# Kernel optimization log

Hardware: AMD Instinct MI355X
Metric: run time of the kernel (lower is better)

The kernel has to match this reference:

```python
import jax, jax.numpy as jnp
import numpy as np

T, B = 16, 32
C, H, W = 3, 120, 160
NET, LSTM_H, AC_H, NACT = 512, 512, 512, 8
CONV_OUT = 64 * 11 * 16  # 11264, from 120x160 through k[8,4,3]/s[4,2,1]


def setup_inputs() -> dict:
    key = jax.random.key(0)
    ks = jax.random.split(key, 32)
    rn = lambda k, shape, s=0.05: jax.random.normal(k, shape, jnp.float32) * s
    return {
        "x": jax.random.normal(ks[0], (T * B, C, H, W), jnp.float32),
        "done": jax.random.randint(ks[1], (T * B,), 0, 2, jnp.int32),
        "h0": rn(ks[2], (1, B, LSTM_H), 1.0),
        "c0": rn(ks[3], (1, B, LSTM_H), 1.0),
        "w1": rn(ks[4], (32, C, 8, 8)), "b1": jnp.zeros((32,), jnp.float32),
        "w2": rn(ks[5], (64, 32, 4, 4)), "b2": jnp.zeros((64,), jnp.float32),
        "w3": rn(ks[6], (64, 64, 3, 3)), "b3": jnp.zeros((64,), jnp.float32),
        "fcW": rn(ks[7], (NET, CONV_OUT), 0.01), "fcb": jnp.zeros((NET,), jnp.float32),
        "Wih": rn(ks[8], (4 * LSTM_H, NET)), "Whh": rn(ks[9], (4 * LSTM_H, LSTM_H)),
        "bih": jnp.zeros((4 * LSTM_H,), jnp.float32), "bhh": jnp.zeros((4 * LSTM_H,), jnp.float32),
        "A1": rn(ks[10], (AC_H, LSTM_H)), "Ab1": jnp.zeros((AC_H,), jnp.float32),
        "A2": rn(ks[11], (NACT, AC_H)), "Ab2": jnp.zeros((NACT,), jnp.float32),
        "C1": rn(ks[12], (AC_H, LSTM_H)), "Cb1": jnp.zeros((AC_H,), jnp.float32),
        "C2": rn(ks[13], (1, AC_H)), "Cb2": jnp.zeros((1,), jnp.float32),
    }


DN = ("NCHW", "OIHW", "NCHW")


def _conv(x, w, b, s):
    y = jax.lax.conv_general_dilated(x, w, (s, s), "VALID", dimension_numbers=DN)
    return y + b[None, :, None, None]


def reference(x, done, h0, c0, w1, b1, w2, b2, w3, b3, fcW, fcb,
              Wih, Whh, bih, bhh, A1, Ab1, A2, Ab2, C1, Cb1, C2, Cb2):
    # CNN feature extractor
    h = jax.nn.relu(_conv(x, w1, b1, 4))
    h = jax.nn.relu(_conv(h, w2, b2, 2))
    h = jax.nn.relu(_conv(h, w3, b3, 1))
    h = h.reshape(h.shape[0], -1)                     # [T*B, CONV_OUT]
    h = jax.nn.leaky_relu(h @ fcW.T + fcb, 0.2)       # [T*B, NET]

    bsz = h0.shape[1]
    xs = h.reshape(-1, bsz, Wih.shape[1])             # [T, B, NET]
    d = done.astype(h.dtype).reshape(-1, bsz)         # [T, B]

    def step(carry, inp):
        hs, cs = carry
        xt, dt = inp
        m = (1.0 - dt)[:, None]                       # done-mask reset
        hs, cs = hs * m, cs * m
        g = xt @ Wih.T + bih + hs @ Whh.T + bhh       # [B, 4H], gate order i,f,g,o
        i, f, gg, o = jnp.split(g, 4, axis=-1)
        cs = jax.nn.sigmoid(f) * cs + jax.nn.sigmoid(i) * jnp.tanh(gg)
        hs = jax.nn.sigmoid(o) * jnp.tanh(cs)
        return (hs, cs), hs

    (hT, cT), outs = jax.lax.scan(step, (h0[0], c0[0]), (xs, d))
    nh = outs.reshape(-1, outs.shape[-1])             # [T*B, LSTM_H]

    a = jax.nn.leaky_relu(nh @ A1.T + Ab1, 0.01)
    logits = a @ A2.T + Ab2                           # [T*B, NACT]
    v = jax.nn.leaky_relu(nh @ C1.T + Cb1, 0.01)
    value = v @ C2.T + Cb2                            # [T*B, 1]
    return logits, value, hT[None], cT[None]
```

## Files before the change

### kernel.cpp

```cpp
#include <hip/hip_runtime.h>
#include <hip/hip_bf16.h>
#include <math.h>

using short8 = __attribute__((ext_vector_type(8))) short;
using f32x4  = __attribute__((ext_vector_type(4))) float;
typedef unsigned long long u64;

#define MFMA16(a, b, c) __builtin_amdgcn_mfma_f32_16x16x32_bf16(a, b, c, 0, 0, 0)

__device__ __forceinline__ short f2bs(float f) {
    __hip_bfloat16 h = __float2bfloat16(f);
    return __builtin_bit_cast(short, h);
}
__device__ __forceinline__ float bs2f(short s) {
    return __uint_as_float(((unsigned)(unsigned short)s) << 16);
}

__global__ void __launch_bounds__(256) k_megaprep(
        const float* __restrict__ w1, const float* __restrict__ w2,
        const float* __restrict__ w3, const float* __restrict__ fcW,
        const float* __restrict__ Wih, const float* __restrict__ Whh,
        const float* __restrict__ A1, const float* __restrict__ C1,
        const float* __restrict__ A2, const float* __restrict__ C2,
        const float* __restrict__ h0, const int* __restrict__ done,
        const float* __restrict__ bih, const float* __restrict__ bhh,
        const float* __restrict__ Ab1, const float* __restrict__ Cb1,
        short* __restrict__ wc1, short* __restrict__ wc2, short* __restrict__ wc3,
        short* __restrict__ fcwr, short* __restrict__ wihb, short* __restrict__ whhb,
        short* __restrict__ a1b, short* __restrict__ c1b, short* __restrict__ a2b,
        short* __restrict__ c2b, short* __restrict__ hm0,
        float* __restrict__ bias2, float* __restrict__ biasAC, unsigned* __restrict__ flags) {
    __shared__ short t[176 * 76];
    const int bid = blockIdx.x, tid = threadIdx.x;

    auto cvt4 = [&](const float* in, short* out, int i) {
        float4 v = *(const float4*)(in + i * 4);
        out[i * 4 + 0] = f2bs(v.x); out[i * 4 + 1] = f2bs(v.y);
        out[i * 4 + 2] = f2bs(v.z); out[i * 4 + 3] = f2bs(v.w);
    };

    if (bid < 512) {
        int r = bid;
        for (int it = 0; it < 11; ++it) {
            int c4 = it * 256 + tid;
            float4 v = *(const float4*)(fcW + (size_t)r * 11264 + c4 * 4);
            int c = c4 * 4;
            int oc = c / 176, pix = c % 176;
            t[(pix + 0) * 76 + oc] = f2bs(v.x);
            t[(pix + 1) * 76 + oc] = f2bs(v.y);
            t[(pix + 2) * 76 + oc] = f2bs(v.z);
            t[(pix + 3) * 76 + oc] = f2bs(v.w);
        }
        __syncthreads();
        for (int it = 0; it < 6; ++it) {
            int j8 = it * 256 + tid;
            if (j8 < 1408) {
                int j = j8 * 8, pix = j >> 6, oc0 = j & 63;
                const short* tp = &t[pix * 76 + oc0];
                short8 v;
                ((uint2*)&v)[0] = *(const uint2*)tp;
                ((uint2*)&v)[1] = *(const uint2*)(tp + 4);
                *(short8*)&fcwr[(size_t)r * 11264 + j] = v;
            }
        }
    } else if (bid < 1536) {
        cvt4(Wih, wihb, (bid - 512) * 256 + tid);
    } else if (bid < 2560) {
        cvt4(Whh, whhb, (bid - 1536) * 256 + tid);
    } else if (bid < 2816) {
        cvt4(A1, a1b, (bid - 2560) * 256 + tid);
    } else if (bid < 3072) {
        cvt4(C1, c1b, (bid - 2816) * 256 + tid);
    } else if (bid < 3078) {
        cvt4(w1, wc1, (bid - 3072) * 256 + tid);
    } else if (bid < 3206) {
        int i = (bid - 3078) * 256 + tid;
        int oc = i >> 9, col = i & 511;
        int kh = col >> 7, kw = (col >> 5) & 3, ic = col & 31;
        wc2[i] = f2bs(w2[((oc * 32 + ic) * 4 + kh) * 4 + kw]);
    } else if (bid < 3350) {
        int i = (bid - 3206) * 256 + tid;
        int oc = i / 576, col = i % 576;
        int kh = col / 192, r = col % 192, kw = r >> 6, ic = r & 63;
        wc3[i] = f2bs(w3[((oc * 64 + ic) * 3 + kh) * 3 + kw]);
    } else if (bid < 3354) {
        cvt4(A2, a2b, (bid - 3350) * 256 + tid);
    } else if (bid < 3355) {
        if (tid < 128) cvt4(C2, c2b, tid);
    } else if (bid < 3419) {
        int i = (bid - 3355) * 256 + tid;
        float m = 1.f - (float)done[i >> 9];
        hm0[i] = f2bs(h0[i] * m);
    } else if (bid < 3427) {
        int i = (bid - 3419) * 256 + tid;
        bias2[i] = bih[i] + bhh[i];
    } else if (bid < 3431) {
        int i = (bid - 3427) * 256 + tid;
        biasAC[i] = (i < 512) ? Ab1[i] : Cb1[i - 512];
    } else {
        if (tid < 16) flags[tid] = 0u;
    }
}

__global__ void __launch_bounds__(256) k_conv123(
        const float* __restrict__ x,   const short* __restrict__ Wc1,
        const float* __restrict__ b1,
        const short* __restrict__ Wc2, const float* __restrict__ b2,
        const short* __restrict__ Wc3, const float* __restrict__ b3,
        short* __restrict__ y3) {
    __shared__ short img1[36192];
    __shared__ short img2[14976];
    __shared__ short ct[2048];
    const int n = blockIdx.x, tid = threadIdx.x;
    const int w = tid >> 6, l = tid & 63, lr = l & 15, lg = l >> 4;
    const int par = w >> 1, nfh = w & 1;

    {
        short8 bf[6][2];
#pragma unroll
        for (int ks = 0; ks < 6; ++ks)
#pragma unroll
            for (int nf = 0; nf < 2; ++nf)
                bf[ks][nf] = *(const short8*)&Wc1[(nf * 16 + lr) * 192 + ks * 32 + lg * 8];
        const float bc0 = b1[lr], bc1 = b1[16 + lr];
        const float* xb = x + (size_t)n * 57600;
        auto tileBase = [&](int tt) -> const float* {
            int p = tt * 16 + lr; if (p > 1130) p = 1130;
            int oh = p / 39, ow = p - oh * 39;
            return xb + (oh * 4) * 160 + ow * 4;
        };
        const int ntiles = (w == 3) ? 17 : 18;
        float4 fA[6][2], fB[6][2];
        {
            const float* base = tileBase(w);
#pragma unroll
            for (int ks = 0; ks < 6; ++ks) {
                int ic = ks >> 1, kh = (ks & 1) * 4 + lg;
                const float* ap = base + ic * 19200 + kh * 160;
                fA[ks][0] = *(const float4*)ap;
                fA[ks][1] = *(const float4*)(ap + 4);
            }
        }
        for (int i = 0; i < ntiles; ++i) {
            const int tt = i * 4 + w;
            if (i + 1 < ntiles) {
                const float* nb = tileBase(tt + 4);
#pragma unroll
                for (int ks = 0; ks < 6; ++ks) {
                    int ic = ks >> 1, kh = (ks & 1) * 4 + lg;
                    const float* ap = nb + ic * 19200 + kh * 160;
                    fB[ks][0] = *(const float4*)ap;
                    fB[ks][1] = *(const float4*)(ap + 4);
                }
            }
            f32x4 acc[2] = {};
#pragma unroll
            for (int ks = 0; ks < 6; ++ks) {
                short8 a;
                a[0] = f2bs(fA[ks][0].x); a[1] = f2bs(fA[ks][0].y);
                a[2] = f2bs(fA[ks][0].z); a[3] = f2bs(fA[ks][0].w);
                a[4] = f2bs(fA[ks][1].x); a[5] = f2bs(fA[ks][1].y);
                a[6] = f2bs(fA[ks][1].z); a[7] = f2bs(fA[ks][1].w);
                acc[0] = MFMA16(a, bf[ks][0], acc[0]);
                acc[1] = MFMA16(a, bf[ks][1], acc[1]);
            }
#pragma unroll
            for (int j = 0; j < 4; ++j) {
                ct[w * 512 + (lg * 4 + j) * 32 + lr] = f2bs(fmaxf(acc[0][j] + bc0, 0.f));
                ct[w * 512 + (lg * 4 + j) * 32 + 16 + lr] = f2bs(fmaxf(acc[1][j] + bc1, 0.f));
            }
            asm volatile("s_waitcnt lgkmcnt(0)" ::: "memory");
            {
                int row = l >> 2, c8 = (l & 3) * 8;
                int pg = tt * 16 + row;
                if (pg < 1131) {
                    short8 v = *(const short8*)&ct[w * 512 + row * 32 + c8];
                    int b = pg * 64 + c8 * 2;
                    b ^= ((b >> 7) & 7) << 4;
                    *(short8*)((char*)img1 + b) = v;
                }
            }
            asm volatile("s_waitcnt lgkmcnt(0)" ::: "memory");
            if (i + 1 < ntiles) {
#pragma unroll
                for (int ks = 0; ks < 6; ++ks) {
                    fA[ks][0] = fB[ks][0];
                    fA[ks][1] = fB[ks][1];
                }
            }
        }
    }
    __syncthreads();

    {
        short8 bfg[16][2];
#pragma unroll
        for (int ks = 0; ks < 16; ++ks)
#pragma unroll
            for (int q2 = 0; q2 < 2; ++q2)
                bfg[ks][q2] = *(const short8*)&Wc2[(nfh * 32 + q2 * 16 + lr) * 512 + ks * 32 + lg * 8];
        float bc[2] = {b2[nfh * 32 + lr], b2[nfh * 32 + 16 + lr]};
        for (int t = par; t < 16; t += 2) {
            int p = t * 16 + lr;
            int pc = p < 234 ? p : 233;
            int oh = pc / 18, ow = pc - oh * 18;
            int base = (oh * 2 * 39 + ow * 2) * 64 + lg * 16;
            f32x4 acc[2] = {};
#pragma unroll
            for (int ks = 0; ks < 16; ++ks) {
                int kh = ks >> 2, kw = ks & 3;
                int b = base + (kh * 39 + kw) * 64;
                b ^= ((b >> 7) & 7) << 4;
                short8 a = *(const short8*)((const char*)img1 + b);
                acc[0] = MFMA16(a, bfg[ks][0], acc[0]);
                acc[1] = MFMA16(a, bfg[ks][1], acc[1]);
            }
#pragma unroll
            for (int q2 = 0; q2 < 2; ++q2)
#pragma unroll
                for (int j = 0; j < 4; ++j)
                    ct[par * 1024 + (lg * 4 + j) * 64 + nfh * 32 + q2 * 16 + lr] =
                        f2bs(fmaxf(acc[q2][j] + bc[q2], 0.f));
            __syncthreads();
            int li = nfh * 64 + l;
            int row = li >> 3, c8 = (li & 7) * 8;
            short8 v = *(const short8*)&ct[par * 1024 + row * 64 + c8];
            int pg = t * 16 + row;
            if (pg < 234) {
                int b = (pg * 64 + c8) * 2;
                b ^= ((b >> 7) & 7) << 4;
                *(short8*)((char*)img2 + b) = v;
            }
            __syncthreads();
        }
    }
    __syncthreads();

    {
        short8 bfg[18][2];
#pragma unroll
        for (int ks = 0; ks < 18; ++ks)
#pragma unroll
            for (int q2 = 0; q2 < 2; ++q2)
                bfg[ks][q2] = *(const short8*)&Wc3[(nfh * 32 + q2 * 16 + lr) * 576 + ks * 32 + lg * 8];
        float bc[2] = {b3[nfh * 32 + lr], b3[nfh * 32 + 16 + lr]};
        for (int t = par; t < 12; t += 2) {
            int p = t * 16 + lr;
            int pc = p < 176 ? p : 175;
            int oh = pc >> 4, ow = pc & 15;
            int base = (oh * 18 + ow) * 128 + lg * 16;
            f32x4 acc[2] = {};
#pragma unroll
            for (int ks = 0; ks < 18; ++ks) {
                int kh = ks / 6, r6 = ks % 6, kw = r6 >> 1, ich = r6 & 1;
                int b = base + (kh * 18 + kw) * 128 + ich * 64;
                b ^= ((b >> 7) & 7) << 4;
                short8 a = *(const short8*)((const char*)img2 + b);
                acc[0] = MFMA16(a, bfg[ks][0], acc[0]);
                acc[1] = MFMA16(a, bfg[ks][1], acc[1]);
            }
#pragma unroll
            for (int q2 = 0; q2 < 2; ++q2)
#pragma unroll
                for (int j = 0; j < 4; ++j)
                    ct[par * 1024 + (lg * 4 + j) * 64 + nfh * 32 + q2 * 16 + lr] =
                        f2bs(fmaxf(acc[q2][j] + bc[q2], 0.f));
            __syncthreads();
            int li = nfh * 64 + l;
            int row = li >> 3, c8 = (li & 7) * 8;
            short8 v = *(const short8*)&ct[par * 1024 + row * 64 + c8];
            int pg = t * 16 + row;
            if (pg < 176)
                *(short8*)&y3[((size_t)n * 176 + pg) * 64 + c8] = v;
            __syncthreads();
        }
    }
}

__global__ void k_gemm_mfma(const short* __restrict__ A, const short* __restrict__ W,
                            float* __restrict__ part, int M, int N, int K, int kPerSplit) {
    __shared__ short As[2][64 * 40];
    __shared__ short Ws[2][64 * 40];
    const int tid = threadIdx.x;
    const int m0 = blockIdx.y * 64, n0 = blockIdx.x * 64;
    const int k0s = blockIdx.z * kPerSplit, k0e = k0s + kPerSplit;
    const int w = tid >> 6, l = tid & 63;
    const int wr = w >> 1, wc = w & 1;
    const int sr = tid >> 2, sc = tid & 3;
    const int lr = l & 15, lg = l >> 4;
    f32x4 acc[2][2] = {};
    for (int k0 = k0s; k0 < k0e; k0 += 64) {
        short8 av0 = *(const short8*)(A + (size_t)(m0 + sr) * K + k0 + sc * 8);
        short8 av1 = *(const short8*)(A + (size_t)(m0 + sr) * K + k0 + 32 + sc * 8);
        short8 wv0 = *(const short8*)(W + (size_t)(n0 + sr) * K + k0 + sc * 8);
        short8 wv1 = *(const short8*)(W + (size_t)(n0 + sr) * K + k0 + 32 + sc * 8);
        __syncthreads();
        *(short8*)&As[0][sr * 40 + sc * 8] = av0;
        *(short8*)&As[1][sr * 40 + sc * 8] = av1;
        *(short8*)&Ws[0][sr * 40 + sc * 8] = wv0;
        *(short8*)&Ws[1][sr * 40 + sc * 8] = wv1;
        __syncthreads();
        int cb = lg * 8;
#pragma unroll
        for (int h = 0; h < 2; ++h) {
            short8 a0 = *(const short8*)&As[h][(wr * 32 + lr) * 40 + cb];
            short8 a1 = *(const short8*)&As[h][(wr * 32 + 16 + lr) * 40 + cb];
            short8 b0 = *(const short8*)&Ws[h][(wc * 32 + lr) * 40 + cb];
            short8 b1 = *(const short8*)&Ws[h][(wc * 32 + 16 + lr) * 40 + cb];
            acc[0][0] = MFMA16(a0, b0, acc[0][0]);
            acc[0][1] = MFMA16(a0, b1, acc[0][1]);
            acc[1][0] = MFMA16(a1, b0, acc[1][0]);
            acc[1][1] = MFMA16(a1, b1, acc[1][1]);
        }
    }
    float* pp = part + (size_t)blockIdx.z * M * N;
#pragma unroll
    for (int mi = 0; mi < 2; ++mi)
#pragma unroll
        for (int ni = 0; ni < 2; ++ni)
#pragma unroll
            for (int j = 0; j < 4; ++j) {
                int row = m0 + wr * 32 + mi * 16 + lg * 4 + j;
                int col = n0 + wc * 32 + ni * 16 + lr;
                pp[(size_t)row * N + col] = acc[mi][ni][j];
            }
}

__global__ void k_epilogue(const float* __restrict__ part, const float* __restrict__ bias,
                           short* __restrict__ out_b, float* __restrict__ out_f,
                           int MN, int N, int S, float slope) {
    int i = (blockIdx.x * 256 + threadIdx.x) * 4;
    if (i >= MN) return;
    float4 v = *(const float4*)(part + i);
    for (int s = 1; s < S; ++s) {
        float4 p = *(const float4*)(part + (size_t)s * MN + i);
        v.x += p.x; v.y += p.y; v.z += p.z; v.w += p.w;
    }
    float4 b = *(const float4*)(bias + (i % N));
    v.x += b.x; v.y += b.y; v.z += b.z; v.w += b.w;
    v.x = (v.x >= 0.f) ? v.x : v.x * slope;
    v.y = (v.y >= 0.f) ? v.y : v.y * slope;
    v.z = (v.z >= 0.f) ? v.z : v.z * slope;
    v.w = (v.w >= 0.f) ? v.w : v.w * slope;
    if (out_b) {
        out_b[i + 0] = f2bs(v.x); out_b[i + 1] = f2bs(v.y);
        out_b[i + 2] = f2bs(v.z); out_b[i + 3] = f2bs(v.w);
    }
    if (out_f) *(float4*)(out_f + i) = v;
}

__global__ void k_gemm_bias(const short* __restrict__ A, const short* __restrict__ W,
                            const float* __restrict__ bias, short* __restrict__ out_b,
                            float* __restrict__ out_f, int M, int N, int K, float slope) {
    __shared__ short As[2][64 * 40];
    __shared__ short Ws[2][64 * 40];
    const int tid = threadIdx.x;
    const int m0 = blockIdx.y * 64, n0 = blockIdx.x * 64;
    const int w = tid >> 6, l = tid & 63;
    const int wr = w >> 1, wc = w & 1;
    const int sr = tid >> 2, sc = tid & 3;
    const int lr = l & 15, lg = l >> 4;
    f32x4 acc[2][2] = {};
    for (int k0 = 0; k0 < K; k0 += 64) {
        short8 av0 = *(const short8*)(A + (size_t)(m0 + sr) * K + k0 + sc * 8);
        short8 av1 = *(const short8*)(A + (size_t)(m0 + sr) * K + k0 + 32 + sc * 8);
        short8 wv0 = *(const short8*)(W + (size_t)(n0 + sr) * K + k0 + sc * 8);
        short8 wv1 = *(const short8*)(W + (size_t)(n0 + sr) * K + k0 + 32 + sc * 8);
        __syncthreads();
        *(short8*)&As[0][sr * 40 + sc * 8] = av0;
        *(short8*)&As[1][sr * 40 + sc * 8] = av1;
        *(short8*)&Ws[0][sr * 40 + sc * 8] = wv0;
        *(short8*)&Ws[1][sr * 40 + sc * 8] = wv1;
        __syncthreads();
        int cb = lg * 8;
#pragma unroll
        for (int h = 0; h < 2; ++h) {
            short8 a0 = *(const short8*)&As[h][(wr * 32 + lr) * 40 + cb];
            short8 a1 = *(const short8*)&As[h][(wr * 32 + 16 + lr) * 40 + cb];
            short8 b0 = *(const short8*)&Ws[h][(wc * 32 + lr) * 40 + cb];
            short8 b1 = *(const short8*)&Ws[h][(wc * 32 + 16 + lr) * 40 + cb];
            acc[0][0] = MFMA16(a0, b0, acc[0][0]);
            acc[0][1] = MFMA16(a0, b1, acc[0][1]);
            acc[1][0] = MFMA16(a1, b0, acc[1][0]);
            acc[1][1] = MFMA16(a1, b1, acc[1][1]);
        }
    }
#pragma unroll
    for (int mi = 0; mi < 2; ++mi)
#pragma unroll
        for (int ni = 0; ni < 2; ++ni)
#pragma unroll
            for (int j = 0; j < 4; ++j) {
                int row = m0 + wr * 32 + mi * 16 + lg * 4 + j;
                int col = n0 + wc * 32 + ni * 16 + lr;
                float v = acc[mi][ni][j] + bias[col];
                v = (v >= 0.f) ? v : v * slope;
                if (out_f) out_f[(size_t)row * N + col] = v;
                else       out_b[(size_t)row * N + col] = f2bs(v);
            }
}

__global__ void __launch_bounds__(1024) k_lstm_all4(
        const float* __restrict__ P, const short* __restrict__ Whhb,
        const int* __restrict__ done, u64* __restrict__ hq0, u64* __restrict__ hq1,
        const float* __restrict__ c0, short* __restrict__ nh,
        float* __restrict__ outH, float* __restrict__ outC, unsigned* __restrict__ flags) {
    __shared__ short hs[32 * 520];
    __shared__ float gb[4 * 32 * 33];
    __shared__ short ch[32 * 33];
    const int b = blockIdx.x;
    const int tid = threadIdx.x;
    const int w = tid >> 6, l = tid & 63, lr = l & 15, lg = l >> 4;
    const int mt = w & 1, nt = w >> 1;
    const int r = nt * 16 + lr;
    const int gate = r >> 5, ul = r & 31;
    const int G = gate * 512 + b * 32 + ul;
    short8 bfg[16];
    const short* wrow = Whhb + (size_t)G * 512;
#pragma unroll
    for (int ks = 0; ks < 16; ++ks) bfg[ks] = *(const short8*)(wrow + ks * 32 + lg * 8);
    const int cu = tid >> 5, cb = tid & 31;
    float cr = c0[cb * 512 + b * 32 + cu];
    const int pb = tid >> 3;
    unsigned dmC = 0, dmP = 0;
#pragma unroll
    for (int q = 0; q < 16; ++q) {
        dmC |= (done[q * 32 + cb] ? 1u : 0u) << q;
        dmP |= (done[q * 32 + pb] ? 1u : 0u) << q;
    }
    float pr[4];
#pragma unroll
    for (int j = 0; j < 4; ++j)
        pr[j] = P[(size_t)(mt * 16 + lg * 4 + j) * 2048 + G];

    for (int t = 0; t < 16; ++t) {
        const u64* hin = (t & 1) ? hq1 : hq0;
        u64* hout      = (t & 1) ? hq0 : hq1;
        if (t > 0) {
            if (tid < 16) {
                while (__hip_atomic_load(flags + tid, __ATOMIC_RELAXED,
                                         __HIP_MEMORY_SCOPE_AGENT) < (unsigned)t)
                    __builtin_amdgcn_s_sleep(1);
            }
            __syncthreads();
        }
#pragma unroll
        for (int it = 0; it < 4; ++it) {
            int i = it * 1024 + tid;
            u64 g = __hip_atomic_load(hin + i, __ATOMIC_RELAXED, __HIP_MEMORY_SCOPE_AGENT);
            *(u64*)&hs[(i >> 7) * 520 + (i & 127) * 4] = g;
        }
        __syncthreads();
        f32x4 acc = {};
#pragma unroll
        for (int ks = 0; ks < 16; ++ks) {
            short8 a = *(const short8*)&hs[(mt * 16 + lr) * 520 + ks * 32 + lg * 8];
            acc = MFMA16(a, bfg[ks], acc);
        }
#pragma unroll
        for (int j = 0; j < 4; ++j)
            gb[gate * 1056 + ul * 33 + (mt * 16 + lg * 4 + j)] = acc[j] + pr[j];
        __syncthreads();
        {
            float gi = gb[0 * 1056 + cu * 33 + cb];
            float gf = gb[1 * 1056 + cu * 33 + cb];
            float gg = gb[2 * 1056 + cu * 33 + cb];
            float go = gb[3 * 1056 + cu * 33 + cb];
            float m = ((dmC >> t) & 1u) ? 0.f : 1.f;
            float ig = 1.f / (1.f + expf(-gi));
            float fg = 1.f / (1.f + expf(-gf));
            float gt = tanhf(gg);
            float og = 1.f / (1.f + expf(-go));
            float cn = fg * (cr * m) + ig * gt;
            float hn = og * tanhf(cn);
            cr = cn;
            ch[cu * 33 + cb] = f2bs(hn);
            if (t == 15) {
                outH[cb * 512 + b * 32 + cu] = hn;
                outC[cb * 512 + b * 32 + cu] = cn;
            }
        }
        __syncthreads();
        if (t < 15) {
            if (tid < 256) {
                int bb3 = tid >> 3, uq = (tid & 7) * 4;
                u64 q = 0;
                if (!((dmP >> (t + 1)) & 1u)) {
                    unsigned lo = ((unsigned)(unsigned short)ch[uq * 33 + bb3]) |
                                  (((unsigned)(unsigned short)ch[(uq + 1) * 33 + bb3]) << 16);
                    unsigned hi = ((unsigned)(unsigned short)ch[(uq + 2) * 33 + bb3]) |
                                  (((unsigned)(unsigned short)ch[(uq + 3) * 33 + bb3]) << 16);
                    q = (u64)lo | ((u64)hi << 32);
                }
                __hip_atomic_store(hout + bb3 * 128 + b * 8 + (tid & 7), q,
                                   __ATOMIC_RELAXED, __HIP_MEMORY_SCOPE_AGENT);
            }
            asm volatile("s_waitcnt vmcnt(0)" ::: "memory");
            __syncthreads();
            if (tid == 0)
                __hip_atomic_store(flags + b, (unsigned)(t + 1),
                                   __ATOMIC_RELAXED, __HIP_MEMORY_SCOPE_AGENT);
        }
        if (tid < 512) {
            int bb2 = tid >> 4, up = (tid & 15) * 2;
            unsigned pkv = ((unsigned)(unsigned short)ch[up * 33 + bb2]) |
                           (((unsigned)(unsigned short)ch[(up + 1) * 33 + bb2]) << 16);
            *(unsigned*)&nh[(size_t)(t * 32 + bb2) * 512 + b * 32 + up] = pkv;
        }
        int tp = (t < 15) ? t + 1 : 15;
#pragma unroll
        for (int j = 0; j < 4; ++j)
            pr[j] = P[(size_t)(tp * 32 + mt * 16 + lg * 4 + j) * 2048 + G];
    }
}

__global__ void k_heads(const short* __restrict__ aAC,
                        const short* __restrict__ A2b, const float* __restrict__ Ab2,
                        const short* __restrict__ C2b, const float* __restrict__ Cb2,
                        float* __restrict__ out) {
    int idx = blockIdx.x * 4 + (threadIdx.x >> 6);
    int l = threadIdx.x & 63;
    if (idx >= 4608) return;
    int row = idx / 9, col = idx % 9;
    const short* act = aAC + (size_t)row * 1024 + (col < 8 ? 0 : 512);
    const short* wr  = (col < 8) ? (A2b + (size_t)col * 512) : C2b;
    short8 a = *(const short8*)(act + l * 8);
    short8 wv = *(const short8*)(wr + l * 8);
    float s = 0.f;
#pragma unroll
    for (int q = 0; q < 8; ++q) s += bs2f(a[q]) * bs2f(wv[q]);
#pragma unroll
    for (int off = 32; off > 0; off >>= 1) s += __shfl_xor(s, off, 64);
    if (l == 0) {
        if (col < 8) out[row * 8 + col] = s + Ab2[col];
        else out[4096 + row] = s + Cb2[0];
    }
}


extern "C" void kernel_launch(void* const* d_in, const int* in_sizes, int n_in,
                              void* d_out, int out_size, void* d_ws, size_t ws_size,
                              hipStream_t stream) {
    (void)in_sizes; (void)n_in; (void)out_size; (void)ws_size;
    const float* x    = (const float*)d_in[0];
    const int*   done = (const int*)  d_in[1];
    const float* h0   = (const float*)d_in[2];
    const float* c0   = (const float*)d_in[3];
    const float* w1   = (const float*)d_in[4];
    const float* b1   = (const float*)d_in[5];
    const float* w2   = (const float*)d_in[6];
    const float* b2   = (const float*)d_in[7];
    const float* w3   = (const float*)d_in[8];
    const float* b3   = (const float*)d_in[9];
    const float* fcW  = (const float*)d_in[10];
    const float* fcb  = (const float*)d_in[11];
    const float* Wih  = (const float*)d_in[12];
    const float* Whh  = (const float*)d_in[13];
    const float* bih  = (const float*)d_in[14];
    const float* bhh  = (const float*)d_in[15];
    const float* A1   = (const float*)d_in[16];
    const float* Ab1  = (const float*)d_in[17];
    const float* A2   = (const float*)d_in[18];
    const float* Ab2  = (const float*)d_in[19];
    const float* C1   = (const float*)d_in[20];
    const float* Cb1  = (const float*)d_in[21];
    const float* C2   = (const float*)d_in[22];
    const float* Cb2  = (const float*)d_in[23];
    float* out = (float*)d_out;

    char* wsp = (char*)d_ws;
    auto alloc = [&](size_t bytes) {
        char* p = wsp; wsp += (bytes + 255) & ~(size_t)255; return p;
    };
    short* a3s  = (short*)alloc(5767168ull * 2);
    short* hfc  = (short*)alloc(262144ull * 2);
    float* P    = (float*)alloc(1048576ull * 4);
    short* whhb = (short*)alloc(1048576ull * 2);
    u64*   hq0  = (u64*)  alloc(16384ull * 2);
    u64*   hq1  = (u64*)  alloc(16384ull * 2);
    short* nh   = (short*)alloc(262144ull * 2);
    short* aAC  = (short*)alloc(524288ull * 2);
    float* part = (float*)alloc(2097152ull * 4);
    short* wc1  = (short*)alloc(6144ull * 2);
    short* wc2  = (short*)alloc(32768ull * 2);
    short* wc3  = (short*)alloc(36864ull * 2);
    short* fcwr = (short*)alloc(5767168ull * 2);
    short* wihb = (short*)alloc(1048576ull * 2);
    short* a1b  = (short*)alloc(262144ull * 2);
    short* c1b  = (short*)alloc(262144ull * 2);
    short* a2b  = (short*)alloc(4096ull * 2);
    short* c2b  = (short*)alloc(512ull * 2);
    float* bias2  = (float*)alloc(2048ull * 4);
    float* biasAC = (float*)alloc(1024ull * 4);
    unsigned* flags = (unsigned*)alloc(256);

    k_megaprep<<<3432, 256, 0, stream>>>(w1, w2, w3, fcW, Wih, Whh, A1, C1, A2, C2,
                                         h0, done, bih, bhh, Ab1, Cb1,
                                         wc1, wc2, wc3, fcwr, wihb, whhb,
                                         a1b, c1b, a2b, c2b, (short*)hq0,
                                         bias2, biasAC, flags);

    k_conv123<<<512, 256, 0, stream>>>(x, wc1, b1, wc2, b2, wc3, b3, a3s);

    k_gemm_mfma<<<dim3(8, 8, 8), 256, 0, stream>>>(a3s, fcwr, part, 512, 512, 11264, 1408);
    k_epilogue<<<256, 256, 0, stream>>>(part, fcb, hfc, nullptr, 262144, 512, 8, 0.2f);

    k_gemm_bias<<<dim3(32, 8), 256, 0, stream>>>(hfc, wihb, bias2, nullptr, P,
                                                 512, 2048, 512, 1.0f);

    k_lstm_all4<<<16, 1024, 0, stream>>>(P, whhb, done, hq0, hq1, c0, nh,
                                         out + 4608, out + 20992, flags);

    k_gemm_bias<<<dim3(16, 8), 256, 0, stream>>>(nh, a1b, biasAC, aAC, nullptr,
                                                 512, 1024, 512, 0.01f);
    k_heads<<<1152, 256, 0, stream>>>(aAC, a2b, Ab2, c2b, Cb2, out);
}
```

Baseline: 194.3 us.

## Replace full conv1 LDS image with 16-row ring buffer processed in two phases

Result: slower. 207.4 us (+6.7%).

```diff
diff --git a/kernel.cpp b/kernel.cpp
--- a/kernel.cpp
+++ b/kernel.cpp
@@ -108,31 +108,33 @@
         const short* __restrict__ Wc2, const float* __restrict__ b2,
         const short* __restrict__ Wc3, const float* __restrict__ b3,
         short* __restrict__ y3) {
-    __shared__ short img1[36192];
+    __shared__ short ring[19968];
     __shared__ short img2[14976];
     __shared__ short ct[2048];
     const int n = blockIdx.x, tid = threadIdx.x;
     const int w = tid >> 6, l = tid & 63, lr = l & 15, lg = l >> 4;
     const int par = w >> 1, nfh = w & 1;
 
-    {
-        short8 bf[6][2];
-#pragma unroll
-        for (int ks = 0; ks < 6; ++ks)
-#pragma unroll
-            for (int nf = 0; nf < 2; ++nf)
-                bf[ks][nf] = *(const short8*)&Wc1[(nf * 16 + lr) * 192 + ks * 32 + lg * 8];
-        const float bc0 = b1[lr], bc1 = b1[16 + lr];
-        const float* xb = x + (size_t)n * 57600;
+    short8 bf1[6][2];
+#pragma unroll
+    for (int ks = 0; ks < 6; ++ks)
+#pragma unroll
+        for (int nf = 0; nf < 2; ++nf)
+            bf1[ks][nf] = *(const short8*)&Wc1[(nf * 16 + lr) * 192 + ks * 32 + lg * 8];
+    const float bc10 = b1[lr], bc11 = b1[16 + lr];
+    const float* xb = x + (size_t)n * 57600;
+
+    auto conv1_tiles = [&](int tstart, int tcount) {
         auto tileBase = [&](int tt) -> const float* {
             int p = tt * 16 + lr; if (p > 1130) p = 1130;
             int oh = p / 39, ow = p - oh * 39;
             return xb + (oh * 4) * 160 + ow * 4;
         };
-        const int ntiles = (w == 3) ? 17 : 18;
+        const int nt = (tcount - w + 3) >> 2;
+        if (nt <= 0) return;
         float4 fA[6][2], fB[6][2];
         {
-            const float* base = tileBase(w);
+            const float* base = tileBase(tstart + w);
 #pragma unroll
             for (int ks = 0; ks < 6; ++ks) {
                 int ic = ks >> 1, kh = (ks & 1) * 4 + lg;
@@ -141,9 +143,9 @@
                 fA[ks][1] = *(const float4*)(ap + 4);
             }
         }
-        for (int i = 0; i < ntiles; ++i) {
-            const int tt = i * 4 + w;
-            if (i + 1 < ntiles) {
+        for (int i = 0; i < nt; ++i) {
+            const int tt = tstart + w + i * 4;
+            if (i + 1 < nt) {
                 const float* nb = tileBase(tt + 4);
 #pragma unroll
                 for (int ks = 0; ks < 6; ++ks) {
@@ -161,13 +163,13 @@
                 a[2] = f2bs(fA[ks][0].z); a[3] = f2bs(fA[ks][0].w);
                 a[4] = f2bs(fA[ks][1].x); a[5] = f2bs(fA[ks][1].y);
                 a[6] = f2bs(fA[ks][1].z); a[7] = f2bs(fA[ks][1].w);
-                acc[0] = MFMA16(a, bf[ks][0], acc[0]);
-                acc[1] = MFMA16(a, bf[ks][1], acc[1]);
+                acc[0] = MFMA16(a, bf1[ks][0], acc[0]);
+                acc[1] = MFMA16(a, bf1[ks][1], acc[1]);
             }
 #pragma unroll
             for (int j = 0; j < 4; ++j) {
-                ct[w * 512 + (lg * 4 + j) * 32 + lr] = f2bs(fmaxf(acc[0][j] + bc0, 0.f));
-                ct[w * 512 + (lg * 4 + j) * 32 + 16 + lr] = f2bs(fmaxf(acc[1][j] + bc1, 0.f));
+                ct[w * 512 + (lg * 4 + j) * 32 + lr] = f2bs(fmaxf(acc[0][j] + bc10, 0.f));
+                ct[w * 512 + (lg * 4 + j) * 32 + 16 + lr] = f2bs(fmaxf(acc[1][j] + bc11, 0.f));
             }
             asm volatile("s_waitcnt lgkmcnt(0)" ::: "memory");
             {
@@ -175,13 +177,14 @@
                 int pg = tt * 16 + row;
                 if (pg < 1131) {
                     short8 v = *(const short8*)&ct[w * 512 + row * 32 + c8];
-                    int b = pg * 64 + c8 * 2;
+                    int prow = pg / 39, pcol = pg - prow * 39;
+                    int b = ((prow & 15) * 39 + pcol) * 64 + c8 * 2;
                     b ^= ((b >> 7) & 7) << 4;
-                    *(short8*)((char*)img1 + b) = v;
+                    *(short8*)((char*)ring + b) = v;
                 }
             }
             asm volatile("s_waitcnt lgkmcnt(0)" ::: "memory");
-            if (i + 1 < ntiles) {
+            if (i + 1 < nt) {
 #pragma unroll
                 for (int ks = 0; ks < 6; ++ks) {
                     fA[ks][0] = fB[ks][0];
@@ -189,10 +192,9 @@
                 }
             }
         }
-    }
-    __syncthreads();
-
-    {
+    };
+
+    auto conv2_tiles = [&](int pxbase, int pxlast) {
         short8 bfg[16][2];
 #pragma unroll
         for (int ks = 0; ks < 16; ++ks)
@@ -200,18 +202,18 @@
             for (int q2 = 0; q2 < 2; ++q2)
                 bfg[ks][q2] = *(const short8*)&Wc2[(nfh * 32 + q2 * 16 + lr) * 512 + ks * 32 + lg * 8];
         float bc[2] = {b2[nfh * 32 + lr], b2[nfh * 32 + 16 + lr]};
-        for (int t = par; t < 16; t += 2) {
-            int p = t * 16 + lr;
-            int pc = p < 234 ? p : 233;
+        for (int t = par; t < 8; t += 2) {
+            int p = pxbase + t * 16 + lr;
+            int pc = p < pxlast ? p : pxlast;
             int oh = pc / 18, ow = pc - oh * 18;
-            int base = (oh * 2 * 39 + ow * 2) * 64 + lg * 16;
             f32x4 acc[2] = {};
 #pragma unroll
             for (int ks = 0; ks < 16; ++ks) {
                 int kh = ks >> 2, kw = ks & 3;
-                int b = base + (kh * 39 + kw) * 64;
+                int row = oh * 2 + kh;
+                int b = ((row & 15) * 39 + ow * 2 + kw) * 64 + lg * 16;
                 b ^= ((b >> 7) & 7) << 4;
-                short8 a = *(const short8*)((const char*)img1 + b);
+                short8 a = *(const short8*)((const char*)ring + b);
                 acc[0] = MFMA16(a, bfg[ks][0], acc[0]);
                 acc[1] = MFMA16(a, bfg[ks][1], acc[1]);
             }
@@ -225,15 +227,23 @@
             int li = nfh * 64 + l;
             int row = li >> 3, c8 = (li & 7) * 8;
             short8 v = *(const short8*)&ct[par * 1024 + row * 64 + c8];
-            int pg = t * 16 + row;
-            if (pg < 234) {
+            int pg = pxbase + t * 16 + row;
+            if (pg <= pxlast) {
                 int b = (pg * 64 + c8) * 2;
                 b ^= ((b >> 7) & 7) << 4;
                 *(short8*)((char*)img2 + b) = v;
             }
             __syncthreads();
         }
-    }
+    };
+
+    conv1_tiles(0, 39);
+    __syncthreads();
+    conv2_tiles(0, 125);
+    __syncthreads();
+    conv1_tiles(39, 32);
+    __syncthreads();
+    conv2_tiles(126, 233);
     __syncthreads();
 
     {
```

## Split fused conv kernel spatially into three row bands per image

Applied to the files above, without the earlier changes.

Result: slower. 226.9 us (+16.8%).

```diff
diff --git a/kernel.cpp b/kernel.cpp
--- a/kernel.cpp
+++ b/kernel.cpp
@@ -108,12 +108,21 @@
         const short* __restrict__ Wc2, const float* __restrict__ b2,
         const short* __restrict__ Wc3, const float* __restrict__ b3,
         short* __restrict__ y3) {
-    __shared__ short img1[36192];
-    __shared__ short img2[14976];
+    __shared__ short a1buf[17472];
+    __shared__ short a2buf[6912];
     __shared__ short ct[2048];
-    const int n = blockIdx.x, tid = threadIdx.x;
+    const int bid = blockIdx.x;
+    const int part = bid >> 9, n = bid & 511;
+    const int tid = threadIdx.x;
     const int w = tid >> 6, l = tid & 63, lr = l & 15, lg = l >> 4;
     const int par = w >> 1, nfh = w & 1;
+
+    const int r0  = (part == 0) ? 0 : (part == 1) ? 8 : 16;
+    const int nr1 = (part == 2) ? 12 : 14;
+    const int c0  = (part == 0) ? 0 : (part == 1) ? 4 : 8;
+    const int nc2 = (part == 2) ? 5 : 6;
+    const int d0  = (part == 0) ? 0 : (part == 1) ? 4 : 8;
+    const int nd3 = (part == 2) ? 3 : 4;
 
     {
         short8 bf[6][2];
@@ -124,68 +133,72 @@
                 bf[ks][nf] = *(const short8*)&Wc1[(nf * 16 + lr) * 192 + ks * 32 + lg * 8];
         const float bc0 = b1[lr], bc1 = b1[16 + lr];
         const float* xb = x + (size_t)n * 57600;
+        const int px1 = nr1 * 39;
+        const int ntile1 = (px1 + 15) >> 4;
         auto tileBase = [&](int tt) -> const float* {
-            int p = tt * 16 + lr; if (p > 1130) p = 1130;
-            int oh = p / 39, ow = p - oh * 39;
-            return xb + (oh * 4) * 160 + ow * 4;
+            int lp = tt * 16 + lr; if (lp > px1 - 1) lp = px1 - 1;
+            int lrow = lp / 39, lcol = lp - lrow * 39;
+            return xb + ((r0 + lrow) * 4) * 160 + lcol * 4;
         };
-        const int ntiles = (w == 3) ? 17 : 18;
-        float4 fA[6][2], fB[6][2];
-        {
-            const float* base = tileBase(w);
-#pragma unroll
-            for (int ks = 0; ks < 6; ++ks) {
-                int ic = ks >> 1, kh = (ks & 1) * 4 + lg;
-                const float* ap = base + ic * 19200 + kh * 160;
-                fA[ks][0] = *(const float4*)ap;
-                fA[ks][1] = *(const float4*)(ap + 4);
-            }
-        }
-        for (int i = 0; i < ntiles; ++i) {
-            const int tt = i * 4 + w;
-            if (i + 1 < ntiles) {
-                const float* nb = tileBase(tt + 4);
+        const int nt = (ntile1 - w + 3) >> 2;
+        if (nt > 0) {
+            float4 fA[6][2], fB[6][2];
+            {
+                const float* base = tileBase(w);
 #pragma unroll
                 for (int ks = 0; ks < 6; ++ks) {
                     int ic = ks >> 1, kh = (ks & 1) * 4 + lg;
-                    const float* ap = nb + ic * 19200 + kh * 160;
-                    fB[ks][0] = *(const float4*)ap;
-                    fB[ks][1] = *(const float4*)(ap + 4);
+                    const float* ap = base + ic * 19200 + kh * 160;
+                    fA[ks][0] = *(const float4*)ap;
+                    fA[ks][1] = *(const float4*)(ap + 4);
                 }
             }
-            f32x4 acc[2] = {};
-#pragma unroll
-            for (int ks = 0; ks < 6; ++ks) {
-                short8 a;
-                a[0] = f2bs(fA[ks][0].x); a[1] = f2bs(fA[ks][0].y);
-                a[2] = f2bs(fA[ks][0].z); a[3] = f2bs(fA[ks][0].w);
-                a[4] = f2bs(fA[ks][1].x); a[5] = f2bs(fA[ks][1].y);
-                a[6] = f2bs(fA[ks][1].z); a[7] = f2bs(fA[ks][1].w);
-                acc[0] = MFMA16(a, bf[ks][0], acc[0]);
-                acc[1] = MFMA16(a, bf[ks][1], acc[1]);
-            }
-#pragma unroll
-            for (int j = 0; j < 4; ++j) {
-                ct[w * 512 + (lg * 4 + j) * 32 + lr] = f2bs(fmaxf(acc[0][j] + bc0, 0.f));
-                ct[w * 512 + (lg * 4 + j) * 32 + 16 + lr] = f2bs(fmaxf(acc[1][j] + bc1, 0.f));
-            }
-            asm volatile("s_waitcnt lgkmcnt(0)" ::: "memory");
-            {
-                int row = l >> 2, c8 = (l & 3) * 8;
-                int pg = tt * 16 + row;
-                if (pg < 1131) {
-                    short8 v = *(const short8*)&ct[w * 512 + row * 32 + c8];
-                    int b = pg * 64 + c8 * 2;
-                    b ^= ((b >> 7) & 7) << 4;
-                    *(short8*)((char*)img1 + b) = v;
+            for (int i = 0; i < nt; ++i) {
+                const int tt = i * 4 + w;
+                if (i + 1 < nt) {
+                    const float* nb = tileBase(tt + 4);
+#pragma unroll
+                    for (int ks = 0; ks < 6; ++ks) {
+                        int ic = ks >> 1, kh = (ks & 1) * 4 + lg;
+                        const float* ap = nb + ic * 19200 + kh * 160;
+                        fB[ks][0] = *(const float4*)ap;
+                        fB[ks][1] = *(const float4*)(ap + 4);
+                    }
                 }
-            }
-            asm volatile("s_waitcnt lgkmcnt(0)" ::: "memory");
-            if (i + 1 < ntiles) {
+                f32x4 acc[2] = {};
 #pragma unroll
                 for (int ks = 0; ks < 6; ++ks) {
-                    fA[ks][0] = fB[ks][0];
-                    fA[ks][1] = fB[ks][1];
+                    short8 a;
+                    a[0] = f2bs(fA[ks][0].x); a[1] = f2bs(fA[ks][0].y);
+                    a[2] = f2bs(fA[ks][0].z); a[3] = f2bs(fA[ks][0].w);
+                    a[4] = f2bs(fA[ks][1].x); a[5] = f2bs(fA[ks][1].y);
+                    a[6] = f2bs(fA[ks][1].z); a[7] = f2bs(fA[ks][1].w);
+                    acc[0] = MFMA16(a, bf[ks][0], acc[0]);
+                    acc[1] = MFMA16(a, bf[ks][1], acc[1]);
+                }
+#pragma unroll
+                for (int j = 0; j < 4; ++j) {
+                    ct[w * 512 + (lg * 4 + j) * 32 + lr] = f2bs(fmaxf(acc[0][j] + bc0, 0.f));
+                    ct[w * 512 + (lg * 4 + j) * 32 + 16 + lr] = f2bs(fmaxf(acc[1][j] + bc1, 0.f));
+                }
+                asm volatile("s_waitcnt lgkmcnt(0)" ::: "memory");
+                {
+                    int row = l >> 2, c8 = (l & 3) * 8;
+                    int pg = tt * 16 + row;
+                    if (pg < px1) {
+                        short8 v = *(const short8*)&ct[w * 512 + row * 32 + c8];
+                        int b = pg * 64 + c8 * 2;
+                        b ^= ((b >> 7) & 7) << 4;
+                        *(short8*)((char*)a1buf + b) = v;
+                    }
+                }
+                asm volatile("s_waitcnt lgkmcnt(0)" ::: "memory");
+                if (i + 1 < nt) {
+#pragma unroll
+                    for (int ks = 0; ks < 6; ++ks) {
+                        fA[ks][0] = fB[ks][0];
+                        fA[ks][1] = fB[ks][1];
+                    }
                 }
             }
         }
@@ -200,18 +213,21 @@
             for (int q2 = 0; q2 < 2; ++q2)
                 bfg[ks][q2] = *(const short8*)&Wc2[(nfh * 32 + q2 * 16 + lr) * 512 + ks * 32 + lg * 8];
         float bc[2] = {b2[nfh * 32 + lr], b2[nfh * 32 + 16 + lr]};
-        for (int t = par; t < 16; t += 2) {
-            int p = t * 16 + lr;
-            int pc = p < 234 ? p : 233;
-            int oh = pc / 18, ow = pc - oh * 18;
-            int base = (oh * 2 * 39 + ow * 2) * 64 + lg * 16;
+        const int px2 = nc2 * 18;
+        const int T2 = ((px2 + 15) >> 4 + 0);
+        const int T2pad = (T2 + 1) & ~1;
+        for (int t = par; t < T2pad; t += 2) {
+            int q = t * 16 + lr;
+            if (q > px2 - 1) q = px2 - 1;
+            int oh = c0 + q / 18, ow = q % 18;
+            int base = ((oh * 2 - r0) * 39 + ow * 2) * 64 + lg * 16;
             f32x4 acc[2] = {};
 #pragma unroll
             for (int ks = 0; ks < 16; ++ks) {
                 int kh = ks >> 2, kw = ks & 3;
                 int b = base + (kh * 39 + kw) * 64;
                 b ^= ((b >> 7) & 7) << 4;
-                short8 a = *(const short8*)((const char*)img1 + b);
+                short8 a = *(const short8*)((const char*)a1buf + b);
                 acc[0] = MFMA16(a, bfg[ks][0], acc[0]);
                 acc[1] = MFMA16(a, bfg[ks][1], acc[1]);
             }
@@ -226,10 +242,10 @@
             int row = li >> 3, c8 = (li & 7) * 8;
             short8 v = *(const short8*)&ct[par * 1024 + row * 64 + c8];
             int pg = t * 16 + row;
-            if (pg < 234) {
+            if (pg < px2) {
                 int b = (pg * 64 + c8) * 2;
                 b ^= ((b >> 7) & 7) << 4;
-                *(short8*)((char*)img2 + b) = v;
+                *(short8*)((char*)a2buf + b) = v;
             }
             __syncthreads();
         }
@@ -244,18 +260,21 @@
             for (int q2 = 0; q2 < 2; ++q2)
                 bfg[ks][q2] = *(const short8*)&Wc3[(nfh * 32 + q2 * 16 + lr) * 576 + ks * 32 + lg * 8];
         float bc[2] = {b3[nfh * 32 + lr], b3[nfh * 32 + 16 + lr]};
-        for (int t = par; t < 12; t += 2) {
-            int p = t * 16 + lr;
-            int pc = p < 176 ? p : 175;
-            int oh = pc >> 4, ow = pc & 15;
-            int base = (oh * 18 + ow) * 128 + lg * 16;
+        const int px3 = nd3 * 16;
+        const int T3 = px3 >> 4;
+        const int T3pad = (T3 + 1) & ~1;
+        for (int t = par; t < T3pad; t += 2) {
+            int q = t * 16 + lr;
+            if (q > px3 - 1) q = px3 - 1;
+            int oh3 = d0 + (q >> 4), ow = q & 15;
+            int base = (((oh3 - c0) * 18 + ow) * 128) + lg * 16;
             f32x4 acc[2] = {};
 #pragma unroll
             for (int ks = 0; ks < 18; ++ks) {
                 int kh = ks / 6, r6 = ks % 6, kw = r6 >> 1, ich = r6 & 1;
                 int b = base + (kh * 18 + kw) * 128 + ich * 64;
                 b ^= ((b >> 7) & 7) << 4;
-                short8 a = *(const short8*)((const char*)img2 + b);
+                short8 a = *(const short8*)((const char*)a2buf + b);
                 acc[0] = MFMA16(a, bfg[ks][0], acc[0]);
                 acc[1] = MFMA16(a, bfg[ks][1], acc[1]);
             }
@@ -270,8 +289,8 @@
             int row = li >> 3, c8 = (li & 7) * 8;
             short8 v = *(const short8*)&ct[par * 1024 + row * 64 + c8];
             int pg = t * 16 + row;
-            if (pg < 176)
-                *(short8*)&y3[((size_t)n * 176 + pg) * 64 + c8] = v;
+            if (pg < px3)
+                *(short8*)&y3[((size_t)n * 176 + d0 * 16 + pg) * 64 + c8] = v;
             __syncthreads();
         }
     }
@@ -600,7 +619,7 @@
                                          a1b, c1b, a2b, c2b, (short*)hq0,
                                          bias2, biasAC, flags);
 
-    k_conv123<<<512, 256, 0, stream>>>(x, wc1, b1, wc2, b2, wc3, b3, a3s);
+    k_conv123<<<1536, 256, 0, stream>>>(x, wc1, b1, wc2, b2, wc3, b3, a3s);
 
     k_gemm_mfma<<<dim3(8, 8, 8), 256, 0, stream>>>(a3s, fcwr, part, 512, 512, 11264, 1408);
     k_epilogue<<<256, 256, 0, stream>>>(part, fcb, hfc, nullptr, 262144, 512, 8, 0.2f);
```
